# Optimization experiments

Hardware: AMD Instinct MI355X
Metric: run time of the kernel (lower is better)

Reference implementation:

```python
import jax, jax.numpy as jnp
import numpy as np

DIM = 512
N = 1024
DIM_HEAD = 64
HEADS = 8
BATCH = 8
SCALE = DIM_HEAD ** -0.5


def setup_inputs() -> dict:
    key = jax.random.key(0)
    ks = jax.random.split(key, 9)
    s = 0.02
    return {
        "x": jax.random.normal(ks[0], (BATCH, N, DIM), dtype=jnp.float32),
        "w_qkv": jax.random.normal(ks[1], (3 * DIM, DIM), dtype=jnp.float32) * s,
        "b_qkv": jax.random.normal(ks[2], (3 * DIM,), dtype=jnp.float32) * s,
        "wq": jax.random.normal(ks[3], (N, DIM_HEAD), dtype=jnp.float32) * s,
        "bq": jax.random.normal(ks[4], (N,), dtype=jnp.float32) * s,
        "wk": jax.random.normal(ks[5], (N, DIM_HEAD), dtype=jnp.float32) * s,
        "bk": jax.random.normal(ks[6], (N,), dtype=jnp.float32) * s,
        "w_out": jax.random.normal(ks[7], (DIM, DIM), dtype=jnp.float32) * s,
        "b_out": jax.random.normal(ks[8], (DIM,), dtype=jnp.float32) * s,
    }


def _split_heads(t):
    # [b, n, h*d] -> [b, h, n, d]
    b, n, _ = t.shape
    return t.reshape(b, n, HEADS, DIM_HEAD).transpose(0, 2, 1, 3)


def reference(x, w_qkv, b_qkv, wq, bq, wk, bk, w_out, b_out):
    # fused QKV projection: [b, n, 3*dim]
    qkv = x @ w_qkv.T + b_qkv
    qo, ko, vo = jnp.split(qkv, 3, axis=-1)
    q, k, v = _split_heads(qo), _split_heads(ko), _split_heads(vo)  # [b,h,n,d]

    # additive-attention stage 1: A = softmax(Wq(q) * scale) over last dim
    A = jax.nn.softmax((jnp.einsum('bhnd,md->bhnm', q, wq) + bq) * SCALE, axis=-1)  # [b,h,n,n]
    q_global = jnp.sum(jnp.einsum('bhnm,bhmd->bhnd', A, q), axis=-1, keepdims=True)  # [b,h,n,1]
    p = q_global * k  # [b,h,n,d]

    # stage 2
    B = jax.nn.softmax((jnp.einsum('bhnd,md->bhnm', p, wk) + bk) * SCALE, axis=-1)  # [b,h,n,n]
    k_global = jnp.sum(jnp.einsum('bhnm,bhmd->bhnd', B, p), axis=-1, keepdims=True)  # [b,h,n,1]

    u = (k_global * v).transpose(0, 2, 1, 3).reshape(x.shape[0], N, DIM)  # [b,n,dim]
    out = u @ w_out.T + b_out + qo
    return out
```

## Files before the change

kernel.cpp:

```cpp
#include <hip/hip_runtime.h>


#define SCL2 0.1803368801f
typedef unsigned short u16;
typedef __attribute__((ext_vector_type(8))) short short8;
typedef __attribute__((ext_vector_type(4))) float f32x4;

#define MFMA16(a, b, c) __builtin_amdgcn_mfma_f32_16x16x32_bf16((a), (b), (c), 0, 0, 0)

__device__ __forceinline__ float bf2f(u16 u) {
    union { unsigned int i; float f; } v; v.i = ((unsigned int)u) << 16; return v.f;
}
__device__ __forceinline__ u16 f2bf(float f) {
    union { float f; unsigned int i; } v; v.f = f;
    unsigned int x = v.i;
    return (u16)((x + 0x7FFFu + ((x >> 16) & 1u)) >> 16);
}

__device__ __forceinline__ void gload16(const u16* g, u16* l) {
    __builtin_amdgcn_global_load_lds(
        (__attribute__((address_space(1))) void*)(void*)g,
        (__attribute__((address_space(3))) void*)l, 16, 0, 0);
}

__global__ __launch_bounds__(256) void conv_kernel(
    const float* __restrict__ w_qkv, const float* __restrict__ w_out,
    const float* __restrict__ wq, const float* __restrict__ wk,
    const float* __restrict__ x, u16* __restrict__ wsb)
{
    const int idx = (blockIdx.x * 256 + threadIdx.x) * 4;
    const float* src; int off;
    if      (idx < 786432)  { src = w_qkv; off = idx; }
    else if (idx < 1048576) { src = w_out; off = idx - 786432; }
    else if (idx < 1114112) { src = wq;    off = idx - 1048576; }
    else if (idx < 1179648) { src = wk;    off = idx - 1114112; }
    else                    { src = x;     off = idx - 1179648; }
    float4 v = *(const float4*)(src + off);
    ushort4 o; o.x = f2bf(v.x); o.y = f2bf(v.y); o.z = f2bf(v.z); o.w = f2bf(v.w);
    *(ushort4*)(wsb + idx) = o;
}

#define MQK 0
#define MVU 1
#define MOUT 2

template <int MODE, int NCT>
__global__ __launch_bounds__(256) void gemm_k(
    const u16* __restrict__ Ab, int lda, int acol,
    const u16* __restrict__ Wb, const float* __restrict__ bias,
    const float* __restrict__ kg, const u16* __restrict__ qkws_ro,
    u16* __restrict__ qkws, float* __restrict__ outp,
    float* __restrict__ qsout, float* __restrict__ ksout)
{
    constexpr int BN = NCT * 16;
    constexpr int CST = BN + 8;
    constexpr int ASZ = 128 * 64;
    constexpr int BSZ = BN * 64;
    constexpr int HALF = ASZ + BSZ;
    constexpr int CELEM = 128 * CST;
    constexpr int SMSZ = (2 * HALF > HALF + CELEM) ? 2 * HALF : HALF + CELEM;
    __shared__ u16 sm[SMSZ];
    u16* const Cb = sm + HALF;

    const int t = threadIdx.x;
    const int w = t >> 6, lane = t & 63, s = lane & 15, quad = lane >> 4;
    const int sx = lane & 7;

    const int nwgy = gridDim.y;
    const int nwg = gridDim.x * nwgy;
    const int flat = blockIdx.y * gridDim.x + blockIdx.x;
    const int swz = (flat & 7) * (nwg >> 3) + (flat >> 3);
    const int by = swz % nwgy, bx = swz / nwgy;
    const int bm = bx * 128, jn0 = by * BN;

    const int r8 = lane >> 3;
    const int c8x = ((lane & 7) ^ r8) << 3;

    f32x4 acc[2][NCT];
#pragma unroll
    for (int i = 0; i < 2; ++i)
#pragma unroll
        for (int j = 0; j < NCT; ++j) acc[i][j] = (f32x4){0.f, 0.f, 0.f, 0.f};

    const u16* ga = Ab + (size_t)(bm + w * 32 + r8) * lda + acol + c8x;
    const u16* gb = Wb + (size_t)(jn0 + w * (NCT * 4) + r8) * 512 + c8x;

    auto stage = [&](int buf, int kt) {
        u16* la = sm + buf * HALF + (w * 32) * 64;
        u16* lb = sm + buf * HALF + ASZ + (w * (NCT * 4)) * 64;
#pragma unroll
        for (int j = 0; j < 4; ++j)
            gload16(ga + (size_t)j * 8 * lda + kt, la + j * 8 * 64);
#pragma unroll
        for (int j = 0; j < NCT / 2; ++j)
            gload16(gb + (size_t)j * 8 * 512 + kt, lb + j * 8 * 64);
    };
    auto compute = [&](int buf) {
        const u16* Ab_ = sm + buf * HALF;
        const u16* Bb_ = Ab_ + ASZ;
#pragma unroll
        for (int kk = 0; kk < 2; ++kk) {
            const int ca = ((kk * 4 + quad) ^ sx) << 3;
            short8 a0 = *(const short8*)&Ab_[(w * 32 + s) * 64 + ca];
            short8 a1 = *(const short8*)&Ab_[(w * 32 + 16 + s) * 64 + ca];
#pragma unroll
            for (int ct = 0; ct < NCT; ++ct) {
                short8 bf = *(const short8*)&Bb_[(ct * 16 + s) * 64 + ca];
                acc[0][ct] = MFMA16(a0, bf, acc[0][ct]);
                acc[1][ct] = MFMA16(a1, bf, acc[1][ct]);
            }
        }
    };

    stage(1, 0);
    __syncthreads();
#pragma unroll
    for (int it = 0; it < 7; ++it) {
        const int cur = 1 - (it & 1);
        stage(1 - cur, 64 * (it + 1));
        __builtin_amdgcn_sched_barrier(0);
        compute(cur);
        __syncthreads();
    }
    compute(0);

    if constexpr (MODE == MOUT) {
#pragma unroll
        for (int mt = 0; mt < 2; ++mt)
#pragma unroll
            for (int ct = 0; ct < NCT; ++ct) {
                const int jn = jn0 + ct * 16 + s;
#pragma unroll
                for (int r = 0; r < 4; ++r) {
                    const int row = bm + w * 32 + mt * 16 + quad * 4 + r;
                    outp[(size_t)row * 512 + jn] =
                        acc[mt][ct][r] + bias[jn] + bf2f(qkws_ro[(size_t)row * 1024 + jn]);
                }
            }
    } else {
        float rsum[2][NCT / 4][4];
        if constexpr (MODE == MQK) {
#pragma unroll
            for (int mt = 0; mt < 2; ++mt)
#pragma unroll
                for (int hg = 0; hg < NCT / 4; ++hg)
#pragma unroll
                    for (int r = 0; r < 4; ++r) rsum[mt][hg][r] = 0.f;
        }
        __syncthreads();
#pragma unroll
        for (int mt = 0; mt < 2; ++mt)
#pragma unroll
            for (int ct = 0; ct < NCT; ++ct) {
                const int jn = jn0 + ct * 16 + s;
                const float bj = bias[jn];
#pragma unroll
                for (int r = 0; r < 4; ++r) {
                    const int rowl = w * 32 + mt * 16 + quad * 4 + r;
                    float v = acc[mt][ct][r] + bj;
                    if constexpr (MODE == MVU) {
                        const int row = bm + rowl;
                        v *= kg[(((row >> 10) * 8 + (jn >> 6)) << 10) | (row & 1023)];
                    }
                    if constexpr (MODE == MQK) rsum[mt][ct >> 2][r] += v;
                    Cb[rowl * CST + ct * 16 + s] = f2bf(v);
                }
            }
        if constexpr (MODE == MQK) {
#pragma unroll
            for (int mt = 0; mt < 2; ++mt)
#pragma unroll
                for (int hg = 0; hg < NCT / 4; ++hg)
#pragma unroll
                    for (int r = 0; r < 4; ++r) {
                        float S = rsum[mt][hg][r];
                        S += __shfl_xor(S, 1);
                        S += __shfl_xor(S, 2);
                        S += __shfl_xor(S, 4);
                        S += __shfl_xor(S, 8);
                        if (s == 0) {
                            const int row = bm + w * 32 + mt * 16 + quad * 4 + r;
                            const int jj = jn0 + hg * 64;
                            float* dst = (jj < 512) ? qsout : ksout;
                            dst[((((row >> 10) << 3) | ((jj >> 6) & 7)) << 10) | (row & 1023)] = S;
                        }
                    }
        }
        __syncthreads();
        const int row = t >> 1, ch = (t & 1) * (NCT * 8);
        u16* dp = qkws + (size_t)(bm + row) * 1024 + (MODE == MVU ? 512 : 0) + jn0 + ch;
#pragma unroll
        for (int i = 0; i < NCT; ++i)
            *(uint4*)(dp + i * 8) = *(const uint4*)&Cb[row * CST + ch + i * 8];
    }
}

template <int STG>
__global__ __launch_bounds__(256) void stage_gemm(
    const u16* __restrict__ qkws, int qcol0,
    const u16* __restrict__ wmb, const float* __restrict__ biasv,
    const float* __restrict__ rowscale,
    const float* __restrict__ wv1, const float* __restrict__ wv2,
    float* __restrict__ outg)
{
    __shared__ u16 sm[24576];
    u16* const As = sm;

    const int t = threadIdx.x;
    const int w = t >> 6, lane = t & 63, s = lane & 15, quad = lane >> 4;
    const int sx = lane & 7;
    const int r8 = lane >> 3;
    const int c8x = ((lane & 7) ^ r8) << 3;

    const int flat = blockIdx.y * gridDim.x + blockIdx.x;
    const int swz = (flat & 7) * 64 + (flat >> 3);
    const int h = swz & 7, bx = swz >> 3;
    const int bm = bx * 128;
    const int bh = ((bm >> 10) << 3) + h;
    const int n0 = bm & 1023;

    const u16* gA = qkws + (size_t)(bm + w * 32 + r8) * 1024 + qcol0 + (h << 6) + c8x;
    const u16* gB = wmb + (size_t)(w * 32 + r8) * 64 + c8x;

    auto stageB = [&](int buf, int c) {
        u16* lb = sm + 8192 + buf * 8192 + (w * 32) * 64;
        const u16* g = gB + (size_t)c * 128 * 64;
#pragma unroll
        for (int j = 0; j < 4; ++j)
            gload16(g + (size_t)j * 8 * 64, lb + j * 8 * 64);
    };

#pragma unroll
    for (int j = 0; j < 4; ++j)
        gload16(gA + (size_t)j * 8 * 1024, As + (w * 32 + j * 8) * 64);
    stageB(1, 0);
    __syncthreads();

    short8 a[2][2];
#pragma unroll
    for (int nt = 0; nt < 2; ++nt)
#pragma unroll
        for (int kk = 0; kk < 2; ++kk)
            a[nt][kk] = *(const short8*)&As[(w * 32 + nt * 16 + s) * 64 + (((kk * 4 + quad) ^ sx) << 3)];

    float rsf[2][4];
#pragma unroll
    for (int nt = 0; nt < 2; ++nt)
#pragma unroll
        for (int r = 0; r < 4; ++r) {
            if constexpr (STG == 2)
                rsf[nt][r] = rowscale[(bh << 10) + n0 + w * 32 + nt * 16 + quad * 4 + r] * SCL2;
            else
                rsf[nt][r] = SCL2;
        }

    float z[2][4] = {}, wacc[2][4] = {};

#pragma unroll 1
    for (int c = 0; c < 8; ++c) {
        const int cur = 1 - (c & 1);
        if (c < 7) stageB(1 - cur, c + 1);
        __builtin_amdgcn_sched_barrier(0);

        const int mb = c * 128;
        float bmv[8], wvv[8];
#pragma unroll
        for (int ct = 0; ct < 8; ++ct) {
            const int m = mb + ct * 16 + s;
            bmv[ct] = biasv[m] * SCL2;
            float wv = wv1[(bh << 10) + m];
            if constexpr (STG == 2) wv *= wv2[(bh << 10) + m];
            wvv[ct] = wv;
        }

        const u16* Bb = sm + 8192 + cur * 8192;
#pragma unroll
        for (int ct = 0; ct < 8; ++ct) {
            const short8 b0 = *(const short8*)&Bb[(ct * 16 + s) * 64 + ((quad ^ sx) << 3)];
            const short8 b1 = *(const short8*)&Bb[(ct * 16 + s) * 64 + (((4 + quad) ^ sx) << 3)];
#pragma unroll
            for (int nt = 0; nt < 2; ++nt) {
                f32x4 acc = (f32x4){0.f, 0.f, 0.f, 0.f};
                acc = MFMA16(a[nt][0], b0, acc);
                acc = MFMA16(a[nt][1], b1, acc);
#pragma unroll
                for (int r = 0; r < 4; ++r) {
                    const float e = __builtin_amdgcn_exp2f(rsf[nt][r] * acc[r] + bmv[ct]);
                    z[nt][r] += e;
                    wacc[nt][r] += e * wvv[ct];
                }
            }
        }
        __syncthreads();
    }

#pragma unroll
    for (int nt = 0; nt < 2; ++nt)
#pragma unroll
        for (int r = 0; r < 4; ++r) {
            float Z = z[nt][r], W = wacc[nt][r];
            for (int off = 1; off < 16; off <<= 1) {
                Z += __shfl_xor(Z, off);
                W += __shfl_xor(W, off);
            }
            if (s == 0)
                outg[(bh << 10) + n0 + w * 32 + nt * 16 + quad * 4 + r] = W / Z;
        }
}

extern "C" void kernel_launch(void* const* d_in, const int* in_sizes, int n_in,
                              void* d_out, int out_size, void* d_ws, size_t ws_size,
                              hipStream_t stream)
{
    const float* x     = (const float*)d_in[0];
    const float* w_qkv = (const float*)d_in[1];
    const float* b_qkv = (const float*)d_in[2];
    const float* wq    = (const float*)d_in[3];
    const float* bq    = (const float*)d_in[4];
    const float* wk    = (const float*)d_in[5];
    const float* bk    = (const float*)d_in[6];
    const float* w_out = (const float*)d_in[7];
    const float* b_out = (const float*)d_in[8];
    float* out = (float*)d_out;

    float* qs = (float*)d_ws;
    float* ks = qs + 65536;
    float* qg = ks + 65536;
    float* kg = qg + 65536;
    u16* wsb   = (u16*)(kg + 65536);
    u16* wqkvb = wsb;
    u16* woutb = wqkvb + 786432;
    u16* wqb   = woutb + 262144;
    u16* wkb   = wqb + 65536;
    u16* xb    = wkb + 65536;
    u16* qkws  = xb + 4194304;

    conv_kernel<<<5248, 256, 0, stream>>>(w_qkv, w_out, wq, wk, x, wsb);
    gemm_k<MQK, 8><<<dim3(64, 8), 256, 0, stream>>>(
        xb, 512, 0, wqkvb, b_qkv, nullptr, nullptr, qkws, nullptr, qs, ks);
    stage_gemm<1><<<dim3(64, 8), 256, 0, stream>>>(
        qkws, 0, wqb, bq, nullptr, qs, nullptr, qg);
    stage_gemm<2><<<dim3(64, 8), 256, 0, stream>>>(
        qkws, 512, wkb, bk, qg, qg, ks, kg);
    gemm_k<MVU, 4><<<dim3(64, 8), 256, 0, stream>>>(
        xb, 512, 0, wqkvb + (size_t)1024 * 512, b_qkv + 1024, kg, nullptr, qkws,
        nullptr, nullptr, nullptr);
    gemm_k<MOUT, 4><<<dim3(64, 8), 256, 0, stream>>>(
        qkws, 1024, 512, woutb, b_out, nullptr, qkws, nullptr, out, nullptr, nullptr);
}
```

Measured before the change: 173.6 us.

## Split stage_gemm column tiles across two wave groups with 512-thread blocks

Doubles the stage_gemm block to 512 threads (8 waves). Each 128-column chunk of the score matrix is split between two groups of four waves, and each group handles four of the eight column tiles. Partial softmax sums Z and W are combined through shared memory before the final division. This raises waves in flight to hide the exp- and MFMA-bound softmax accumulation, at the cost of an extra reduction, a barrier and more LDS per block.

```diff
diff --git a/kernel.cpp b/kernel.cpp
--- a/kernel.cpp
+++ b/kernel.cpp
@@ -196,7 +196,7 @@
 }
 
 template <int STG>
-__global__ __launch_bounds__(256) void stage_gemm(
+__global__ __launch_bounds__(512) void stage_gemm(
     const u16* __restrict__ qkws, int qcol0,
     const u16* __restrict__ wmb, const float* __restrict__ biasv,
     const float* __restrict__ rowscale,
@@ -204,6 +204,7 @@
     float* __restrict__ outg)
 {
     __shared__ u16 sm[24576];
+    __shared__ float zp[2][128], wp[2][128];
     u16* const As = sm;
 
     const int t = threadIdx.x;
@@ -211,6 +212,8 @@
     const int sx = lane & 7;
     const int r8 = lane >> 3;
     const int c8x = ((lane & 7) ^ r8) << 3;
+    const int wr = w & 3;
+    const int mg = w >> 2;
 
     const int flat = blockIdx.y * gridDim.x + blockIdx.x;
     const int swz = (flat & 7) * 64 + (flat >> 3);
@@ -219,20 +222,20 @@
     const int bh = ((bm >> 10) << 3) + h;
     const int n0 = bm & 1023;
 
-    const u16* gA = qkws + (size_t)(bm + w * 32 + r8) * 1024 + qcol0 + (h << 6) + c8x;
-    const u16* gB = wmb + (size_t)(w * 32 + r8) * 64 + c8x;
+    const u16* gA = qkws + (size_t)(bm + w * 16 + r8) * 1024 + qcol0 + (h << 6) + c8x;
+    const u16* gB = wmb + (size_t)(w * 16 + r8) * 64 + c8x;
 
     auto stageB = [&](int buf, int c) {
-        u16* lb = sm + 8192 + buf * 8192 + (w * 32) * 64;
+        u16* lb = sm + 8192 + buf * 8192 + (w * 16) * 64;
         const u16* g = gB + (size_t)c * 128 * 64;
 #pragma unroll
-        for (int j = 0; j < 4; ++j)
+        for (int j = 0; j < 2; ++j)
             gload16(g + (size_t)j * 8 * 64, lb + j * 8 * 64);
     };
 
 #pragma unroll
-    for (int j = 0; j < 4; ++j)
-        gload16(gA + (size_t)j * 8 * 1024, As + (w * 32 + j * 8) * 64);
+    for (int j = 0; j < 2; ++j)
+        gload16(gA + (size_t)j * 8 * 1024, As + (w * 16 + j * 8) * 64);
     stageB(1, 0);
     __syncthreads();
 
@@ -241,7 +244,7 @@
     for (int nt = 0; nt < 2; ++nt)
 #pragma unroll
         for (int kk = 0; kk < 2; ++kk)
-            a[nt][kk] = *(const short8*)&As[(w * 32 + nt * 16 + s) * 64 + (((kk * 4 + quad) ^ sx) << 3)];
+            a[nt][kk] = *(const short8*)&As[(wr * 32 + nt * 16 + s) * 64 + (((kk * 4 + quad) ^ sx) << 3)];
 
     float rsf[2][4];
 #pragma unroll
@@ -249,12 +252,13 @@
 #pragma unroll
         for (int r = 0; r < 4; ++r) {
             if constexpr (STG == 2)
-                rsf[nt][r] = rowscale[(bh << 10) + n0 + w * 32 + nt * 16 + quad * 4 + r] * SCL2;
+                rsf[nt][r] = rowscale[(bh << 10) + n0 + wr * 32 + nt * 16 + quad * 4 + r] * SCL2;
             else
                 rsf[nt][r] = SCL2;
         }
 
     float z[2][4] = {}, wacc[2][4] = {};
+    const int ct0 = mg * 4;
 
 #pragma unroll 1
     for (int c = 0; c < 8; ++c) {
@@ -262,20 +266,20 @@
         if (c < 7) stageB(1 - cur, c + 1);
         __builtin_amdgcn_sched_barrier(0);
 
-        const int mb = c * 128;
-        float bmv[8], wvv[8];
-#pragma unroll
-        for (int ct = 0; ct < 8; ++ct) {
-            const int m = mb + ct * 16 + s;
-            bmv[ct] = biasv[m] * SCL2;
+        float bmv[4], wvv[4];
+#pragma unroll
+        for (int i = 0; i < 4; ++i) {
+            const int m = c * 128 + (ct0 + i) * 16 + s;
+            bmv[i] = biasv[m] * SCL2;
             float wv = wv1[(bh << 10) + m];
             if constexpr (STG == 2) wv *= wv2[(bh << 10) + m];
-            wvv[ct] = wv;
+            wvv[i] = wv;
         }
 
         const u16* Bb = sm + 8192 + cur * 8192;
 #pragma unroll
-        for (int ct = 0; ct < 8; ++ct) {
+        for (int i = 0; i < 4; ++i) {
+            const int ct = ct0 + i;
             const short8 b0 = *(const short8*)&Bb[(ct * 16 + s) * 64 + ((quad ^ sx) << 3)];
             const short8 b1 = *(const short8*)&Bb[(ct * 16 + s) * 64 + (((4 + quad) ^ sx) << 3)];
 #pragma unroll
@@ -285,9 +289,9 @@
                 acc = MFMA16(a[nt][1], b1, acc);
 #pragma unroll
                 for (int r = 0; r < 4; ++r) {
-                    const float e = __builtin_amdgcn_exp2f(rsf[nt][r] * acc[r] + bmv[ct]);
+                    const float e = __builtin_amdgcn_exp2f(rsf[nt][r] * acc[r] + bmv[i]);
                     z[nt][r] += e;
-                    wacc[nt][r] += e * wvv[ct];
+                    wacc[nt][r] += e * wvv[i];
                 }
             }
         }
@@ -303,9 +307,18 @@
                 Z += __shfl_xor(Z, off);
                 W += __shfl_xor(W, off);
             }
-            if (s == 0)
-                outg[(bh << 10) + n0 + w * 32 + nt * 16 + quad * 4 + r] = W / Z;
-        }
+            if (s == 0) {
+                const int rowl = wr * 32 + nt * 16 + quad * 4 + r;
+                zp[mg][rowl] = Z;
+                wp[mg][rowl] = W;
+            }
+        }
+    __syncthreads();
+    if (t < 128) {
+        const float Z = zp[0][t] + zp[1][t];
+        const float W = wp[0][t] + wp[1][t];
+        outg[(bh << 10) + n0 + t] = W / Z;
+    }
 }
 
 extern "C" void kernel_launch(void* const* d_in, const int* in_sizes, int n_in,
@@ -338,9 +351,9 @@
     conv_kernel<<<5248, 256, 0, stream>>>(w_qkv, w_out, wq, wk, x, wsb);
     gemm_k<MQK, 8><<<dim3(64, 8), 256, 0, stream>>>(
         xb, 512, 0, wqkvb, b_qkv, nullptr, nullptr, qkws, nullptr, qs, ks);
-    stage_gemm<1><<<dim3(64, 8), 256, 0, stream>>>(
+    stage_gemm<1><<<dim3(64, 8), 512, 0, stream>>>(
         qkws, 0, wqb, bq, nullptr, qs, nullptr, qg);
-    stage_gemm<2><<<dim3(64, 8), 256, 0, stream>>>(
+    stage_gemm<2><<<dim3(64, 8), 512, 0, stream>>>(
         qkws, 512, wkb, bk, qg, qg, ks, kg);
     gemm_k<MVU, 4><<<dim3(64, 8), 256, 0, stream>>>(
         xb, 512, 0, wqkvb + (size_t)1024 * 512, b_qkv + 1024, kg, nullptr, qkws,
```

After: 163.2 us. 1.06x faster.
